# Kernel optimization log

Measured on AMD Instinct MI355X. Metric: run time of the kernel, lower is better.

The kernel has to match this reference:

```python
import jax, jax.numpy as jnp
import numpy as np
from jax import lax

N, H, W, C = 4, 256, 256, 128
COUT = 128
BS_IN, BS_OUT, BSTR = 18, 16, 16  # gather block, conv-out block, block stride
N_ACTIVE = 512


def setup_inputs() -> dict:
    key = jax.random.key(0)
    ks = jax.random.split(key, 8)
    x = jax.random.normal(ks[0], (N, H, W, C), dtype=jnp.float32)
    w = jax.random.normal(ks[1], (3, 3, C, COUT), dtype=jnp.float32) * 0.05  # HWIO
    b = jax.random.normal(ks[2], (COUT,), dtype=jnp.float32) * 0.05
    gamma = jax.random.uniform(ks[3], (COUT,), dtype=jnp.float32, minval=0.5, maxval=1.5)
    beta = jax.random.normal(ks[4], (COUT,), dtype=jnp.float32) * 0.1
    mean = jax.random.normal(ks[5], (COUT,), dtype=jnp.float32) * 0.1
    var = jax.random.uniform(ks[6], (COUT,), dtype=jnp.float32, minval=0.5, maxval=1.5)
    # unique active block ids over the N x (H/16) x (W/16) grid -> disjoint scatter targets
    n_blocks = N * (H // BSTR) * (W // BSTR)
    active = jax.random.permutation(ks[7], n_blocks)[:N_ACTIVE].astype(jnp.int32)
    return {"x": x, "w": w, "b": b, "gamma": gamma, "beta": beta,
            "mean": mean, "var": var, "active": active}


def reference(x, w, b, gamma, beta, mean, var, active):
    n_, h_, w_, c_ = x.shape
    nby, nbx = h_ // BSTR, w_ // BSTR
    bn = active // (nby * nbx)
    rem = active % (nby * nbx)
    by = rem // nbx
    bx = rem % nbx

    # --- sparse_gather: overlapping BS_IN x BS_IN input blocks (zero-pad edges) ---
    pad = BS_IN - BS_OUT
    xp = jnp.pad(x, ((0, 0), (0, pad), (0, pad), (0, 0)))
    Hp, Wp = h_ + pad, w_ + pad
    d_in = jnp.arange(BS_IN, dtype=jnp.int32)
    hs = by[:, None] * BSTR + d_in[None, :]            # [Nb, 18]
    ws = bx[:, None] * BSTR + d_in[None, :]            # [Nb, 18]
    gidx = bn[:, None, None] * (Hp * Wp) + hs[:, :, None] * Wp + ws[:, None, :]
    p = xp.reshape(-1, c_)[gidx]                       # [Nb, 18, 18, C]

    # --- dense conv + BN(eval, eps=1e-3) + ReLU on gathered blocks ---
    q = lax.conv_general_dilated(p, w, window_strides=(1, 1), padding='VALID',
                                 dimension_numbers=('NHWC', 'HWIO', 'NHWC'))
    q = q + b
    q = (q - mean) * (gamma * lax.rsqrt(var + 1e-3)) + beta
    q = jax.nn.relu(q)                                 # [Nb, 16, 16, COUT]

    # --- sparse_scatter: write disjoint BS_OUT blocks back into a copy of x ---
    d_out = jnp.arange(BS_OUT, dtype=jnp.int32)
    hso = by[:, None] * BSTR + d_out[None, :]
    wso = bx[:, None] * BSTR + d_out[None, :]
    sidx = bn[:, None, None] * (h_ * w_) + hso[:, :, None] * w_ + wso[:, None, :]
    y = x.reshape(-1, c_).at[sidx.reshape(-1)].set(q.reshape(-1, q.shape[-1]))
    return y.reshape(n_, h_, w_, c_)
```

## Files before the change

kernel.cpp:

```cpp
#include <hip/hip_runtime.h>
#include <hip/hip_bf16.h>

#define H_ 256
#define W_ 256
#define C_ 128
#define NBPOS 1024
#define NACT 512

typedef __bf16 bf16x8 __attribute__((ext_vector_type(8)));
typedef float f32x4 __attribute__((ext_vector_type(4)));

#define SCALE_OFF 294912
#define SHIFT_OFF 295424
#define INACT_OFF 295936

__global__ void prep_w_kernel(const float* __restrict__ w, __bf16* __restrict__ wprep) {
  int o = blockIdx.x * 256 + threadIdx.x;
  int j = o & 7, cout = (o >> 3) & 127, k8 = (o >> 10) & 15, tap = o >> 14;
  wprep[o] = (__bf16)w[((size_t)tap * 128 + k8 * 8 + j) * 128 + cout];
}

__global__ void small_kernel(const float* __restrict__ b, const float* __restrict__ gamma,
                             const float* __restrict__ beta, const float* __restrict__ mean,
                             const float* __restrict__ var, const int* __restrict__ active,
                             float* __restrict__ scale, float* __restrict__ shift,
                             int* __restrict__ inact) {
  __shared__ unsigned mask[32];
  __shared__ int cnt;
  int tid = threadIdx.x;
  if (tid < 32) mask[tid] = 0u;
  if (tid == 0) cnt = 0;
  __syncthreads();
  if (tid < NACT) {
    int a = active[tid];
    atomicOr(&mask[a >> 5], 1u << (a & 31));
  }
  if (tid < 128) {
    float s = gamma[tid] * rsqrtf(var[tid] + 1e-3f);
    scale[tid] = s;
    shift[tid] = (b[tid] - mean[tid]) * s + beta[tid];
  }
  __syncthreads();
  if (!((mask[tid >> 5] >> (tid & 31)) & 1u)) {
    int p = atomicAdd(&cnt, 1);
    inact[p] = tid;
  }
}

__global__ __launch_bounds__(256, 2) void conv_kernel(
    const float* __restrict__ x, const __bf16* __restrict__ wprep,
    const float* __restrict__ scale, const float* __restrict__ shift,
    const int* __restrict__ active, const int* __restrict__ inact,
    float* __restrict__ y) {
  __shared__ unsigned char ldsA[324 * 128];
  __shared__ unsigned char ldsB[2][8192];

  const int tid = threadIdx.x;
  const int lane = tid & 63;
  const int wid = tid >> 6;
  const int aid = active[blockIdx.x];
  const int bn = aid >> 8, by = (aid >> 4) & 15, bx = aid & 15;
  const int h0 = by * 16, w0 = bx * 16;
  const float* xb = x + (size_t)bn * (H_ * W_ * C_);

  const int cid = inact[blockIdx.x];
  const int cn = cid >> 8, cy = (cid >> 4) & 15, cx = cid & 15;
  const size_t cbase4 = ((((size_t)cn * H_ + cy * 16) * W_ + cx * 16) * C_) >> 2;
  const f32x4* __restrict__ xs = (const f32x4*)x;
  f32x4* __restrict__ ys = (f32x4*)y;
  f32x4 cbuf[4];
  auto cidx = [&](int c, int k) -> size_t {
    int lin = (c << 10) + (k << 8) + tid;
    return cbase4 + (size_t)(lin >> 9) * (W_ * C_ / 4) + (lin & 511);
  };
  auto copy_load = [&](int c) {
#pragma unroll
    for (int k = 0; k < 4; ++k) cbuf[k] = __builtin_nontemporal_load(&xs[cidx(c, k)]);
  };
  auto copy_store = [&](int c) {
#pragma unroll
    for (int k = 0; k < 4; ++k) __builtin_nontemporal_store(cbuf[k], &ys[cidx(c, k)]);
  };

  float sc[8], sh[8];
  {
    int col = lane & 15;
#pragma unroll
    for (int nb = 0; nb < 8; ++nb) {
      sc[nb] = scale[nb * 16 + col];
      sh[nb] = shift[nb * 16 + col];
    }
  }

  f32x4 acc[4][8];
  f32x4 zero = {0.f, 0.f, 0.f, 0.f};
#pragma unroll
  for (int i = 0; i < 4; ++i)
#pragma unroll
    for (int j = 0; j < 8; ++j) acc[i][j] = zero;

  const uint4* wp4 = (const uint4*)wprep;
  uint4 t0, t1;
  auto load_t = [&](int u) {
    int ks = u % 18, h = u / 18;
    int tile = ((ks >> 1) << 2) + (h << 1) + (ks & 1);
    t0 = wp4[tile * 512 + tid];
    t1 = wp4[tile * 512 + 256 + tid];
  };
  auto stage = [&](int half) {
    for (int chunk = tid; chunk < 324 * 8; chunk += 256) {
      int s = chunk >> 3, c8 = chunk & 7;
      int iy = s / 18, ix = s - iy * 18;
      int hs = h0 + iy, wsp = w0 + ix;
      float4 f0 = make_float4(0.f, 0.f, 0.f, 0.f), f1 = f0;
      if (hs < H_ && wsp < W_) {
        const float* p = xb + (size_t)(hs * W_ + wsp) * C_ + half * 64 + c8 * 8;
        f0 = *(const float4*)p;
        f1 = *(const float4*)(p + 4);
      }
      bf16x8 v;
      v[0] = (__bf16)f0.x; v[1] = (__bf16)f0.y; v[2] = (__bf16)f0.z; v[3] = (__bf16)f0.w;
      v[4] = (__bf16)f1.x; v[5] = (__bf16)f1.y; v[6] = (__bf16)f1.z; v[7] = (__bf16)f1.w;
      int lin = s * 128 + c8 * 16;
      *(bf16x8*)(&ldsA[lin ^ ((s & 7) << 4)]) = v;
    }
  };

  load_t(0);
  copy_load(0);
  stage(0);
  ((uint4*)ldsB[0])[tid] = t0;
  ((uint4*)ldsB[0])[256 + tid] = t1;
  load_t(1);
  __syncthreads();

  const int koff = (lane >> 4) * 16;
  const int colb = (lane & 15) * 16;
  const int krow = (lane >> 4) * 2048;

  int cc = 0;
  for (int u = 0; u < 36; ++u) {
    if (u == 5 || u == 10 || u == 15 || u == 19 || u == 24 || u == 28 || u == 33) {
      copy_store(cc);
      copy_load(cc + 1);
      ++cc;
    }
    int cur = u & 1;
    if (u < 35) {
      ((uint4*)ldsB[cur ^ 1])[tid] = t0;
      ((uint4*)ldsB[cur ^ 1])[256 + tid] = t1;
      if (u < 34) load_t(u + 2);
    }
    int ks = u % 18;
    int tap = ks >> 1, kch = ks & 1;
    int dyv = tap / 3, dxv = tap - dyv * 3;

    bf16x8 a[4];
#pragma unroll
    for (int mi = 0; mi < 4; ++mi) {
      int srow = (wid * 4 + mi + dyv) * 18 + dxv + (lane & 15);
      int lin = srow * 128 + kch * 64 + koff;
      a[mi] = *(const bf16x8*)(&ldsA[lin ^ ((srow & 7) << 4)]);
    }
    bf16x8 bfr[8];
#pragma unroll
    for (int nb = 0; nb < 8; ++nb)
      bfr[nb] = *(const bf16x8*)(&ldsB[cur][krow + nb * 256 + colb]);
#pragma unroll
    for (int mi = 0; mi < 4; ++mi)
#pragma unroll
      for (int nb = 0; nb < 8; ++nb)
        acc[mi][nb] = __builtin_amdgcn_mfma_f32_16x16x32_bf16(a[mi], bfr[nb], acc[mi][nb], 0, 0, 0);

    __syncthreads();
    if (u == 17) {
      stage(1);
      __syncthreads();
    }
  }
  copy_store(7);

  const int colc = lane & 15;
  float* yb = y + (((size_t)bn * H_ + h0) * W_ + w0) * C_;
#pragma unroll
  for (int mi = 0; mi < 4; ++mi) {
    int oy = wid * 4 + mi;
#pragma unroll
    for (int r = 0; r < 4; ++r) {
      int ox = (lane >> 4) * 4 + r;
      float* yr = yb + ((size_t)oy * W_ + ox) * C_;
#pragma unroll
      for (int nb = 0; nb < 8; ++nb) {
        float v = acc[mi][nb][r] * sc[nb] + sh[nb];
        __builtin_nontemporal_store(fmaxf(v, 0.f), &yr[nb * 16 + colc]);
      }
    }
  }
}

extern "C" void kernel_launch(void* const* d_in, const int* in_sizes, int n_in,
                              void* d_out, int out_size, void* d_ws, size_t ws_size,
                              hipStream_t stream) {
  const float* x     = (const float*)d_in[0];
  const float* w     = (const float*)d_in[1];
  const float* b     = (const float*)d_in[2];
  const float* gamma = (const float*)d_in[3];
  const float* beta  = (const float*)d_in[4];
  const float* mean  = (const float*)d_in[5];
  const float* var   = (const float*)d_in[6];
  const int*   act   = (const int*)d_in[7];
  float* y = (float*)d_out;
  char* ws = (char*)d_ws;
  __bf16* wprep = (__bf16*)ws;
  float* scale = (float*)(ws + SCALE_OFF);
  float* shift = (float*)(ws + SHIFT_OFF);
  int* inact = (int*)(ws + INACT_OFF);

  prep_w_kernel<<<dim3(576), dim3(256), 0, stream>>>(w, wprep);
  small_kernel<<<dim3(1), dim3(1024), 0, stream>>>(b, gamma, beta, mean, var, act,
                                                   scale, shift, inact);
  conv_kernel<<<dim3(NACT), dim3(256), 0, stream>>>(x, wprep, scale, shift, act, inact, y);
}
```

Baseline: 80.25 us.

## Split conv blocks into half-height tiles and move inactive copy to separate kernel

The passthrough copy of inactive blocks moves out of the conv kernel into its own launch, one workgroup per block position, and workgroups covering active blocks exit early. Each active block is now split across two conv workgroups that each compute 8 output rows, which doubles the grid, shrinks LDS use and accumulators, and raises the occupancy hint to 4. In exchange it adds a kernel launch, re-stages the overlapping halo rows and reloads the weights in both halves, and the copy no longer overlaps with MFMA work.

```diff
diff --git a/kernel.cpp b/kernel.cpp
--- a/kernel.cpp
+++ b/kernel.cpp
@@ -12,7 +12,7 @@
 
 #define SCALE_OFF 294912
 #define SHIFT_OFF 295424
-#define INACT_OFF 295936
+#define FLAGS_OFF 295936
 
 __global__ void prep_w_kernel(const float* __restrict__ w, __bf16* __restrict__ wprep) {
   int o = blockIdx.x * 256 + threadIdx.x;
@@ -24,12 +24,10 @@
                              const float* __restrict__ beta, const float* __restrict__ mean,
                              const float* __restrict__ var, const int* __restrict__ active,
                              float* __restrict__ scale, float* __restrict__ shift,
-                             int* __restrict__ inact) {
+                             int* __restrict__ flags) {
   __shared__ unsigned mask[32];
-  __shared__ int cnt;
   int tid = threadIdx.x;
   if (tid < 32) mask[tid] = 0u;
-  if (tid == 0) cnt = 0;
   __syncthreads();
   if (tid < NACT) {
     int a = active[tid];
@@ -41,61 +39,49 @@
     shift[tid] = (b[tid] - mean[tid]) * s + beta[tid];
   }
   __syncthreads();
-  if (!((mask[tid >> 5] >> (tid & 31)) & 1u)) {
-    int p = atomicAdd(&cnt, 1);
-    inact[p] = tid;
-  }
-}
-
-__global__ __launch_bounds__(256, 2) void conv_kernel(
+  flags[tid] = (mask[tid >> 5] >> (tid & 31)) & 1u;
+}
+
+__global__ __launch_bounds__(256) void copy_kernel(const float* __restrict__ x,
+                                                   const int* __restrict__ flags,
+                                                   float* __restrict__ y) {
+  int pb = blockIdx.x;
+  if (flags[pb]) return;
+  int bn = pb >> 8, by = (pb >> 4) & 15, bx = pb & 15;
+  size_t base4 = ((((size_t)bn * H_ + by * 16) * W_ + bx * 16) * C_) >> 2;
+  const f32x4* __restrict__ xs = (const f32x4*)x;
+  f32x4* __restrict__ ys = (f32x4*)y;
+#pragma unroll 4
+  for (int i = 0; i < 32; ++i) {
+    int lin = (i << 8) + threadIdx.x;
+    int row = lin >> 9, rem = lin & 511;
+    size_t idx4 = base4 + (size_t)row * (W_ * C_ / 4) + rem;
+    f32x4 v = xs[idx4];
+    __builtin_nontemporal_store(v, &ys[idx4]);
+  }
+}
+
+__global__ __launch_bounds__(256, 4) void conv_kernel(
     const float* __restrict__ x, const __bf16* __restrict__ wprep,
     const float* __restrict__ scale, const float* __restrict__ shift,
-    const int* __restrict__ active, const int* __restrict__ inact,
-    float* __restrict__ y) {
-  __shared__ unsigned char ldsA[324 * 128];
+    const int* __restrict__ active, float* __restrict__ y) {
+  __shared__ unsigned char ldsA[180 * 128];
   __shared__ unsigned char ldsB[2][8192];
 
   const int tid = threadIdx.x;
   const int lane = tid & 63;
   const int wid = tid >> 6;
-  const int aid = active[blockIdx.x];
+  const int aid = active[blockIdx.x >> 1];
+  const int mh = blockIdx.x & 1;
   const int bn = aid >> 8, by = (aid >> 4) & 15, bx = aid & 15;
   const int h0 = by * 16, w0 = bx * 16;
+  const int hm = h0 + mh * 8;
   const float* xb = x + (size_t)bn * (H_ * W_ * C_);
 
-  const int cid = inact[blockIdx.x];
-  const int cn = cid >> 8, cy = (cid >> 4) & 15, cx = cid & 15;
-  const size_t cbase4 = ((((size_t)cn * H_ + cy * 16) * W_ + cx * 16) * C_) >> 2;
-  const f32x4* __restrict__ xs = (const f32x4*)x;
-  f32x4* __restrict__ ys = (f32x4*)y;
-  f32x4 cbuf[4];
-  auto cidx = [&](int c, int k) -> size_t {
-    int lin = (c << 10) + (k << 8) + tid;
-    return cbase4 + (size_t)(lin >> 9) * (W_ * C_ / 4) + (lin & 511);
-  };
-  auto copy_load = [&](int c) {
-#pragma unroll
-    for (int k = 0; k < 4; ++k) cbuf[k] = __builtin_nontemporal_load(&xs[cidx(c, k)]);
-  };
-  auto copy_store = [&](int c) {
-#pragma unroll
-    for (int k = 0; k < 4; ++k) __builtin_nontemporal_store(cbuf[k], &ys[cidx(c, k)]);
-  };
-
-  float sc[8], sh[8];
-  {
-    int col = lane & 15;
-#pragma unroll
-    for (int nb = 0; nb < 8; ++nb) {
-      sc[nb] = scale[nb * 16 + col];
-      sh[nb] = shift[nb * 16 + col];
-    }
-  }
-
-  f32x4 acc[4][8];
+  f32x4 acc[2][8];
   f32x4 zero = {0.f, 0.f, 0.f, 0.f};
 #pragma unroll
-  for (int i = 0; i < 4; ++i)
+  for (int i = 0; i < 2; ++i)
 #pragma unroll
     for (int j = 0; j < 8; ++j) acc[i][j] = zero;
 
@@ -108,10 +94,10 @@
     t1 = wp4[tile * 512 + 256 + tid];
   };
   auto stage = [&](int half) {
-    for (int chunk = tid; chunk < 324 * 8; chunk += 256) {
-      int s = chunk >> 3, c8 = chunk & 7;
-      int iy = s / 18, ix = s - iy * 18;
-      int hs = h0 + iy, wsp = w0 + ix;
+    for (int u = tid; u < 180 * 8; u += 256) {
+      int s = u >> 3, c8 = u & 7;
+      int pr = s / 18, col = s - pr * 18;
+      int hs = hm + pr, wsp = w0 + col;
       float4 f0 = make_float4(0.f, 0.f, 0.f, 0.f), f1 = f0;
       if (hs < H_ && wsp < W_) {
         const float* p = xb + (size_t)(hs * W_ + wsp) * C_ + half * 64 + c8 * 8;
@@ -127,7 +113,6 @@
   };
 
   load_t(0);
-  copy_load(0);
   stage(0);
   ((uint4*)ldsB[0])[tid] = t0;
   ((uint4*)ldsB[0])[256 + tid] = t1;
@@ -138,13 +123,7 @@
   const int colb = (lane & 15) * 16;
   const int krow = (lane >> 4) * 2048;
 
-  int cc = 0;
   for (int u = 0; u < 36; ++u) {
-    if (u == 5 || u == 10 || u == 15 || u == 19 || u == 24 || u == 28 || u == 33) {
-      copy_store(cc);
-      copy_load(cc + 1);
-      ++cc;
-    }
     int cur = u & 1;
     if (u < 35) {
       ((uint4*)ldsB[cur ^ 1])[tid] = t0;
@@ -155,10 +134,10 @@
     int tap = ks >> 1, kch = ks & 1;
     int dyv = tap / 3, dxv = tap - dyv * 3;
 
-    bf16x8 a[4];
-#pragma unroll
-    for (int mi = 0; mi < 4; ++mi) {
-      int srow = (wid * 4 + mi + dyv) * 18 + dxv + (lane & 15);
+    bf16x8 a[2];
+#pragma unroll
+    for (int mi = 0; mi < 2; ++mi) {
+      int srow = (wid * 2 + mi + dyv) * 18 + dxv + (lane & 15);
       int lin = srow * 128 + kch * 64 + koff;
       a[mi] = *(const bf16x8*)(&ldsA[lin ^ ((srow & 7) << 4)]);
     }
@@ -167,7 +146,7 @@
     for (int nb = 0; nb < 8; ++nb)
       bfr[nb] = *(const bf16x8*)(&ldsB[cur][krow + nb * 256 + colb]);
 #pragma unroll
-    for (int mi = 0; mi < 4; ++mi)
+    for (int mi = 0; mi < 2; ++mi)
 #pragma unroll
       for (int nb = 0; nb < 8; ++nb)
         acc[mi][nb] = __builtin_amdgcn_mfma_f32_16x16x32_bf16(a[mi], bfr[nb], acc[mi][nb], 0, 0, 0);
@@ -178,13 +157,18 @@
       __syncthreads();
     }
   }
-  copy_store(7);
 
   const int colc = lane & 15;
-  float* yb = y + (((size_t)bn * H_ + h0) * W_ + w0) * C_;
-#pragma unroll
-  for (int mi = 0; mi < 4; ++mi) {
-    int oy = wid * 4 + mi;
+  float sc[8], sh[8];
+#pragma unroll
+  for (int nb = 0; nb < 8; ++nb) {
+    sc[nb] = scale[nb * 16 + colc];
+    sh[nb] = shift[nb * 16 + colc];
+  }
+  float* yb = y + (((size_t)bn * H_ + hm) * W_ + w0) * C_;
+#pragma unroll
+  for (int mi = 0; mi < 2; ++mi) {
+    int oy = wid * 2 + mi;
 #pragma unroll
     for (int r = 0; r < 4; ++r) {
       int ox = (lane >> 4) * 4 + r;
@@ -214,10 +198,11 @@
   __bf16* wprep = (__bf16*)ws;
   float* scale = (float*)(ws + SCALE_OFF);
   float* shift = (float*)(ws + SHIFT_OFF);
-  int* inact = (int*)(ws + INACT_OFF);
+  int* flags = (int*)(ws + FLAGS_OFF);
 
   prep_w_kernel<<<dim3(576), dim3(256), 0, stream>>>(w, wprep);
   small_kernel<<<dim3(1), dim3(1024), 0, stream>>>(b, gamma, beta, mean, var, act,
-                                                   scale, shift, inact);
-  conv_kernel<<<dim3(NACT), dim3(256), 0, stream>>>(x, wprep, scale, shift, act, inact, y);
-}
+                                                   scale, shift, flags);
+  copy_kernel<<<dim3(NBPOS), dim3(256), 0, stream>>>(x, flags, y);
+  conv_kernel<<<dim3(NACT * 2), dim3(256), 0, stream>>>(x, wprep, scale, shift, act, y);
+}
```

Measured after the change: 79.70 us. Within noise of the previous version (-0.7%).
